# Kernel tuning notes

Hardware: AMD Instinct MI355X
Metric: run time of the kernel (lower is better)

The kernel has to match this reference:

```python
import jax, jax.numpy as jnp
import numpy as np

D_MODEL = 512
NUM_HEADS = 8
D_K = D_MODEL // NUM_HEADS
D_FF = 4 * D_MODEL
EPS = 1e-5


def _pos_encoding(seq_len, d_model, dtype=jnp.float32):
    pos = jnp.arange(seq_len, dtype=jnp.float32)[:, None]              # [S,1]
    div = jnp.exp(jnp.arange(0, d_model, 2, dtype=jnp.float32) * (-np.log(10000.0) / d_model))  # [D/2]
    ang = pos * div                                                      # [S,D/2]
    pe = jnp.stack([jnp.sin(ang), jnp.cos(ang)], axis=-1).reshape(seq_len, d_model)
    return pe.astype(dtype)


def _layernorm(x, g, b):
    mu = jnp.mean(x, axis=-1, keepdims=True)
    var = jnp.mean(jnp.square(x - mu), axis=-1, keepdims=True)
    return (x - mu) * jax.lax.rsqrt(var + EPS) * g + b


def setup_inputs() -> dict:
    key = jax.random.key(0)
    ks = jax.random.split(key, 12)
    B, S, D = 4, 2048, D_MODEL
    s = 1.0 / np.sqrt(D)
    inp = {
        "x": jax.random.normal(ks[0], (B, S, D), jnp.float32),
        "Wq": jax.random.normal(ks[1], (D, D), jnp.float32) * s,
        "bq": jnp.zeros((D,), jnp.float32),
        "Wk": jax.random.normal(ks[2], (D, D), jnp.float32) * s,
        "bk": jnp.zeros((D,), jnp.float32),
        "Wv": jax.random.normal(ks[3], (D, D), jnp.float32) * s,
        "bv": jnp.zeros((D,), jnp.float32),
        "Wo": jax.random.normal(ks[4], (D, D), jnp.float32) * s,
        "bo": jnp.zeros((D,), jnp.float32),
        "g1": jnp.ones((D,), jnp.float32),
        "b1": jnp.zeros((D,), jnp.float32),
        "W_ff1": jax.random.normal(ks[5], (D, D_FF), jnp.float32) * s,
        "b_ff1": jnp.zeros((D_FF,), jnp.float32),
        "W_ff2": jax.random.normal(ks[6], (D_FF, D), jnp.float32) * (1.0 / np.sqrt(D_FF)),
        "b_ff2": jnp.zeros((D,), jnp.float32),
        "g2": jnp.ones((D,), jnp.float32),
        "b2": jnp.zeros((D,), jnp.float32),
    }
    return inp


def reference(x, Wq, bq, Wk, bk, Wv, bv, Wo, bo, g1, b1, W_ff1, b_ff1, W_ff2, b_ff2, g2, b2):
    B, S, D = x.shape
    H, dk = NUM_HEADS, D_K
    # positional encoding (deterministic buffer)
    x = x + _pos_encoding(S, D, x.dtype)[None]
    # projections -> [B,H,S,dk]
    q = (x @ Wq + bq).reshape(B, S, H, dk).transpose(0, 2, 1, 3)
    k = (x @ Wk + bk).reshape(B, S, H, dk).transpose(0, 2, 1, 3)
    v = (x @ Wv + bv).reshape(B, S, H, dk).transpose(0, 2, 1, 3)
    # naive attention: materialized [B,H,S,S] scores (as in original)
    scores = jnp.einsum('bhqd,bhkd->bhqk', q, k) / np.sqrt(dk)
    attn = jax.nn.softmax(scores, axis=-1)
    ctx = jnp.einsum('bhqk,bhkd->bhqd', attn, v)
    ctx = ctx.transpose(0, 2, 1, 3).reshape(B, S, D)
    attn_out = ctx @ Wo + bo
    # residual + LN + FFN + residual + LN
    h = _layernorm(x + attn_out, g1, b1)
    ff = jax.nn.relu(h @ W_ff1 + b_ff1) @ W_ff2 + b_ff2
    return _layernorm(h + ff, g2, b2)
```

## Files before the change

### kernel.cpp

```cpp
#include <hip/hip_runtime.h>

typedef unsigned short u16;
typedef unsigned int u32;
typedef __attribute__((ext_vector_type(8))) short s16x8;
typedef __attribute__((ext_vector_type(2))) float f32x2;
typedef __attribute__((ext_vector_type(4))) float f32x4;
typedef __attribute__((ext_vector_type(16))) float f32x16;
typedef __attribute__((ext_vector_type(2))) u32 u32x2;
typedef __attribute__((ext_vector_type(4))) u32 u32x4;

#define MB (1ull << 20)
#define K1SCALE 0.18033688f

__device__ __forceinline__ u16 f2bf(float f) {
  u32 u = __float_as_uint(f);
  u32 r = (u + 0x7fffu + ((u >> 16) & 1u)) >> 16;
  return (u16)r;
}

__device__ __forceinline__ u32 cvtpk(float lo, float hi) {
  u32 r;
  asm("v_cvt_pk_bf16_f32 %0, %1, %2" : "=v"(r) : "v"(lo), "v"(hi));
  return r;
}

__device__ __forceinline__ f32x2 pk_add(f32x2 a, f32x2 b) {
  f32x2 d;
  asm("v_pk_add_f32 %0, %1, %2" : "=v"(d) : "v"(a), "v"(b));
  return d;
}

__device__ __forceinline__ void gload16(const u16* g, u16* l) {
  __builtin_amdgcn_global_load_lds((const __attribute__((address_space(1))) void*)g,
                                   (__attribute__((address_space(3))) void*)l, 16, 0, 0);
}

__global__ __launch_bounds__(256) void k_prep(const float* __restrict__ x,
                                              float* __restrict__ xf, u16* __restrict__ xb,
                                              const float* __restrict__ Wq, const float* __restrict__ Wk,
                                              const float* __restrict__ Wv, const float* __restrict__ Wo,
                                              const float* __restrict__ Wff1, const float* __restrict__ Wff2,
                                              const float* __restrict__ bq, const float* __restrict__ bk,
                                              const float* __restrict__ bv,
                                              u16* __restrict__ WqkvT, u16* __restrict__ WoT,
                                              u16* __restrict__ Wff1T, u16* __restrict__ Wff2T,
                                              float* __restrict__ bqkv) {
  __shared__ float tile[32][33];
  int bid = blockIdx.x;
  if (bid < 8192) {
    int idx = bid * 256 + threadIdx.x;
    int i2 = idx & 255;
    int srow = (idx >> 8) & 2047;
    float div = __expf((float)i2 * -0.03597789207803196f);
    float ang = (float)srow * div;
    f32x2 xv = *(const f32x2*)&x[(size_t)idx * 2];
    float v0 = xv[0] + __sinf(ang);
    float v1 = xv[1] + __cosf(ang);
    *(f32x2*)&xf[(size_t)idx * 2] = (f32x2){v0, v1};
    *(u32*)&xb[(size_t)idx * 2] = cvtpk(v0, v1);
    return;
  }
  int id = bid - 8192;
  if (id >= 3072) {
    int j = (id - 3072) * 256 + threadIdx.x;
    float v = (j < 512) ? bq[j] * K1SCALE : ((j < 1024) ? bk[j - 512] : bv[j - 1024]);
    bqkv[j] = v;
    return;
  }
  const float* W;
  u16* Wt;
  int K, N, k0, n0;
  float sc = 1.0f;
  if (id < 1024) {
    int mi = id >> 8, t = id & 255;
    K = 512; N = 512;
    k0 = (t & 15) * 32;
    n0 = (t >> 4) * 32;
    if (mi == 0) { W = Wq; Wt = WqkvT; sc = K1SCALE; }
    else if (mi == 1) { W = Wk; Wt = WqkvT + 512 * 512; }
    else if (mi == 2) { W = Wv; Wt = WqkvT + 2 * 512 * 512; }
    else { W = Wo; Wt = WoT; }
  } else if (id < 2048) {
    int t = id - 1024;
    K = 512; N = 2048;
    k0 = (t & 15) * 32;
    n0 = (t >> 4) * 32;
    W = Wff1; Wt = Wff1T;
  } else {
    int t = id - 2048;
    K = 2048; N = 512;
    k0 = (t >> 4) * 32;
    n0 = (t & 15) * 32;
    W = Wff2; Wt = Wff2T;
  }
  int tx = threadIdx.x & 31, ty = threadIdx.x >> 5;
  #pragma unroll
  for (int i = 0; i < 32; i += 8)
    tile[ty + i][tx] = W[(size_t)(k0 + ty + i) * N + n0 + tx];
  __syncthreads();
  #pragma unroll
  for (int i = 0; i < 32; i += 8)
    Wt[(size_t)(n0 + ty + i) * K + k0 + tx] = f2bf(tile[tx][ty + i] * sc);
}

template <int NK, bool RELU, bool QKV, bool F32OUT>
__global__ __launch_bounds__(512, 2) void k_gemm3(const u16* __restrict__ A, const u16* __restrict__ Bt,
                                                  const float* __restrict__ bias, u16* __restrict__ Cb,
                                                  u16* __restrict__ vTout,
                                                  float* __restrict__ Cf0, float* __restrict__ Cf1,
                                                  int N, int lda) {
  constexpr int K = NK * 64;
  __shared__ u16 lA[3][256 * 64];
  __shared__ u16 lB[3][128 * 64];
  int t = threadIdx.x;
  int lane = t & 63;
  int w = t >> 6;
  int wr = w >> 1, wc = w & 1;
  int g = lane >> 4, c = lane & 15;
  int nwg = gridDim.x * gridDim.y;
  int fid = blockIdx.y * gridDim.x + blockIdx.x;
  int wid = (fid & 7) * (nwg >> 3) + (fid >> 3);
  int bx = wid / gridDim.y;
  int by = wid % gridDim.y;
  size_t tm = (size_t)bx * 256;
  size_t tn = (size_t)by * 128;
  A += (size_t)blockIdx.z * K;
  Bt += (size_t)blockIdx.z * K;

  auto stg = [&](int buf, int kt, int half) {
    int k0 = kt * 64;
    #pragma unroll
    for (int i = 0; i < 2; i++) {
      int ch = t + (half * 2 + i) * 512;
      int row = ch >> 3;
      int koff = ((ch ^ row) & 7) << 3;
      gload16(A + (tm + row) * lda + k0 + koff, &lA[buf][ch * 8]);
    }
    int ch = t + half * 512;
    int row = ch >> 3;
    int koff = ((ch ^ row) & 7) << 3;
    gload16(Bt + (tn + row) * lda + k0 + koff, &lB[buf][ch * 8]);
  };

  f32x4 acc[4][4];
  #pragma unroll
  for (int i = 0; i < 4; i++)
    #pragma unroll
    for (int j = 0; j < 4; j++) acc[i][j] = (f32x4){0.f, 0.f, 0.f, 0.f};

  stg(0, 0, 0); stg(0, 0, 1);
  stg(1, 1, 0); stg(1, 1, 1);
  asm volatile("s_waitcnt vmcnt(6)" ::: "memory");
  __builtin_amdgcn_s_barrier();
  __builtin_amdgcn_sched_barrier(0);

  #pragma unroll
  for (int kt = 0; kt < NK; kt++) {
    const int buf = kt % 3;
    const int nb = (kt + 2) % 3;
    s16x8 bfr[4][2], afr[2][2];
    #pragma unroll
    for (int nr = 0; nr < 4; nr++)
      #pragma unroll
      for (int ks = 0; ks < 2; ks++)
        bfr[nr][ks] = *(const s16x8*)&lB[buf][(wc * 64 + nr * 16 + c) * 64 + (((g + 4 * ks) ^ (c & 7)) << 3)];
    #pragma unroll
    for (int mr = 0; mr < 2; mr++)
      #pragma unroll
      for (int ks = 0; ks < 2; ks++)
        afr[mr][ks] = *(const s16x8*)&lA[buf][(wr * 64 + mr * 16 + c) * 64 + (((g + 4 * ks) ^ (c & 7)) << 3)];
    if (kt + 2 < NK) stg(nb, kt + 2, 0);
    __builtin_amdgcn_s_barrier();
    __builtin_amdgcn_sched_barrier(0);
    __builtin_amdgcn_s_setprio(1);
    #pragma unroll
    for (int mr = 0; mr < 2; mr++)
      #pragma unroll
      for (int nr = 0; nr < 4; nr++)
        #pragma unroll
        for (int ks = 0; ks < 2; ks++)
          acc[mr][nr] = __builtin_amdgcn_mfma_f32_16x16x32_bf16(afr[mr][ks], bfr[nr][ks], acc[mr][nr], 0, 0, 0);
    __builtin_amdgcn_s_setprio(0);
    __builtin_amdgcn_s_barrier();
    __builtin_amdgcn_sched_barrier(0);
    #pragma unroll
    for (int mr = 0; mr < 2; mr++)
      #pragma unroll
      for (int ks = 0; ks < 2; ks++)
        afr[mr][ks] = *(const s16x8*)&lA[buf][(wr * 64 + (mr + 2) * 16 + c) * 64 + (((g + 4 * ks) ^ (c & 7)) << 3)];
    if (kt + 2 < NK) stg(nb, kt + 2, 1);
    __builtin_amdgcn_s_barrier();
    __builtin_amdgcn_sched_barrier(0);
    __builtin_amdgcn_s_setprio(1);
    #pragma unroll
    for (int mr = 0; mr < 2; mr++)
      #pragma unroll
      for (int nr = 0; nr < 4; nr++)
        #pragma unroll
        for (int ks = 0; ks < 2; ks++)
          acc[mr + 2][nr] = __builtin_amdgcn_mfma_f32_16x16x32_bf16(afr[mr][ks], bfr[nr][ks], acc[mr + 2][nr], 0, 0, 0);
    __builtin_amdgcn_s_setprio(0);
    if (kt < NK - 1) {
      if (kt + 2 < NK)
        asm volatile("s_waitcnt vmcnt(6)" ::: "memory");
      else
        asm volatile("s_waitcnt vmcnt(0)" ::: "memory");
      __builtin_amdgcn_s_barrier();
      __builtin_amdgcn_sched_barrier(0);
    }
  }

  if (QKV && tn >= 1024) {
    #pragma unroll
    for (int mr = 0; mr < 4; mr++) {
      int row0 = (int)tm + wr * 64 + mr * 16 + g * 4;
      int b = row0 >> 11, s0 = row0 & 2047;
      #pragma unroll
      for (int nr = 0; nr < 4; nr++) {
        int colr = (int)(tn - 1024) + wc * 64 + nr * 16 + c;
        int h = colr >> 6, d = colr & 63;
        float bv = bias[1024 + colr];
        u32 w0 = cvtpk(acc[mr][nr][0] + bv, acc[mr][nr][1] + bv);
        u32 w1 = cvtpk(acc[mr][nr][2] + bv, acc[mr][nr][3] + bv);
        u32x2 pp = {w0, w1};
        *(u32x2*)&vTout[((size_t)((b << 3) + h) * 64 + d) * 2048 + s0] = pp;
      }
    }
  } else if (F32OUT) {
    float* Cf = blockIdx.z ? Cf1 : Cf0;
    bool addb = (blockIdx.z == 0);
    #pragma unroll
    for (int nr = 0; nr < 4; nr++) {
      size_t col = tn + wc * 64 + nr * 16 + c;
      float bv = addb ? bias[col] : 0.0f;
      #pragma unroll
      for (int mr = 0; mr < 4; mr++) {
        size_t row0 = tm + wr * 64 + mr * 16 + g * 4;
        #pragma unroll
        for (int r = 0; r < 4; r++) Cf[(row0 + r) * N + col] = acc[mr][nr][r] + bv;
      }
    }
  } else {
    #pragma unroll
    for (int nr = 0; nr < 4; nr++) {
      size_t col = tn + wc * 64 + nr * 16 + c;
      float bv = bias[col];
      #pragma unroll
      for (int mr = 0; mr < 4; mr++) {
        size_t row0 = tm + wr * 64 + mr * 16 + g * 4;
        #pragma unroll
        for (int r = 0; r < 4; r++) {
          float v = acc[mr][nr][r] + bv;
          if (RELU) v = fmaxf(v, 0.0f);
          Cb[(row0 + r) * N + col] = f2bf(v);
        }
      }
    }
  }
}

template <int BN, bool RELU, bool WF32, bool WBF16>
__global__ __launch_bounds__(256) void k_gemm(const u16* __restrict__ A, const u16* __restrict__ Bt,
                                              const float* __restrict__ bias,
                                              float* __restrict__ Cf, u16* __restrict__ Cb,
                                              int N, int K) {
  constexpr int NACC = BN / 32;
  __shared__ u16 lA[128 * 64];
  __shared__ u16 lB[BN * 64];
  int t = threadIdx.x;
  int lane = t & 63;
  int w = t >> 6;
  int wm = w >> 1, wn = w & 1;
  int g = lane >> 4, c = lane & 15;
  int nwg = gridDim.x * gridDim.y;
  int fid = blockIdx.y * gridDim.x + blockIdx.x;
  int wid = (fid & 7) * (nwg >> 3) + (fid >> 3);
  int bx = wid / gridDim.y;
  int by = wid % gridDim.y;
  size_t tm = (size_t)bx * 128;
  size_t tn = (size_t)by * BN;

  f32x4 acc[4][NACC];
  #pragma unroll
  for (int i = 0; i < 4; i++)
    #pragma unroll
    for (int j = 0; j < NACC; j++) acc[i][j] = (f32x4){0.f, 0.f, 0.f, 0.f};

  for (int k0 = 0; k0 < K; k0 += 64) {
    __syncthreads();
    #pragma unroll
    for (int i = 0; i < 4; i++) {
      int ch = t + i * 256;
      int row = ch >> 3;
      int koff = ((ch ^ row) & 7) << 3;
      gload16(A + (tm + row) * K + k0 + koff, lA + ch * 8);
    }
    #pragma unroll
    for (int i = 0; i < BN / 32; i++) {
      int ch = t + i * 256;
      int row = ch >> 3;
      int koff = ((ch ^ row) & 7) << 3;
      gload16(Bt + (tn + row) * K + k0 + koff, lB + ch * 8);
    }
    __syncthreads();
    #pragma unroll
    for (int kh = 0; kh < 2; kh++) {
      int sl = ((g + 4 * kh) ^ (c & 7)) << 3;
      s16x8 af[4], bf[NACC];
      #pragma unroll
      for (int i = 0; i < 4; i++)
        af[i] = *(const s16x8*)&lA[(wm * 64 + i * 16 + c) * 64 + sl];
      #pragma unroll
      for (int j = 0; j < NACC; j++)
        bf[j] = *(const s16x8*)&lB[(wn * (BN / 2) + j * 16 + c) * 64 + sl];
      #pragma unroll
      for (int i = 0; i < 4; i++)
        #pragma unroll
        for (int j = 0; j < NACC; j++)
          acc[i][j] = __builtin_amdgcn_mfma_f32_16x16x32_bf16(af[i], bf[j], acc[i][j], 0, 0, 0);
    }
  }
  #pragma unroll
  for (int j = 0; j < NACC; j++) {
    size_t col = tn + wn * (BN / 2) + j * 16 + c;
    float bv = bias[col];
    #pragma unroll
    for (int i = 0; i < 4; i++) {
      size_t row0 = tm + wm * 64 + i * 16 + g * 4;
      #pragma unroll
      for (int r = 0; r < 4; r++) {
        float v = acc[i][j][r] + bv;
        if (RELU) v = fmaxf(v, 0.0f);
        if (WF32) Cf[(row0 + r) * N + col] = v;
        if (WBF16) Cb[(row0 + r) * N + col] = f2bf(v);
      }
    }
  }
}

union F16U {
  f32x16 v;
  f32x2 p[8];
};

__global__ __launch_bounds__(512, 4) void k_attn(const u16* __restrict__ qkv,
                                                 const u16* __restrict__ vT,
                                                 u16* __restrict__ ctx) {
  __shared__ u16 lds[8][4096];
  int t = threadIdx.x;
  int w = t >> 6, lane = t & 63;
  int qg = w >> 1, kh = w & 1;
  int ql = lane & 31, hi = lane >> 5;
  int bid = blockIdx.x;
  int wid = (bid & 7) * 64 + (bid >> 3);
  int bx = wid & 15;
  int bh = wid >> 4;
  int b = bh >> 3, h = bh & 7;
  int q0 = bx * 128 + qg * 32;
  int r7 = ql & 7;

  int sh = t >> 8;
  int th = t & 255;
  const u16* kbaseg = qkv + (size_t)(b * 2048 + sh * 1024) * 1536 + 512 + h * 64;
  const u16* vbaseg = vT + (size_t)(bh * 64) * 2048 + sh * 1024;

  auto stage = [&](int buf, int step) {
    int t0 = step * 64;
    #pragma unroll
    for (int i = 0; i < 2; i++) {
      int ch = th + i * 256;
      int row = ch >> 3;
      int off = ((ch ^ row) & 7) << 3;
      gload16(kbaseg + (size_t)(t0 + row) * 1536 + off, &lds[(sh * 2 + buf) * 2][ch * 8]);
      gload16(vbaseg + (size_t)row * 2048 + t0 + off, &lds[(sh * 2 + buf) * 2 + 1][ch * 8]);
    }
  };

  const u16* qbase = qkv + (size_t)(b * 2048 + q0 + ql) * 1536 + h * 64 + hi * 8;
  s16x8 qf[4];
  #pragma unroll
  for (int ks = 0; ks < 4; ks++) qf[ks] = *(const s16x8*)(qbase + ks * 16);

  float l = 0.f;
  F16U O0, O1;
  #pragma unroll
  for (int i = 0; i < 16; i++) { O0.v[i] = 0.f; O1.v[i] = 0.f; }

  stage(0, 0);

  for (int step = 0; step < 16; ++step) {
    int buf = step & 1;
    asm volatile("s_waitcnt vmcnt(0)" ::: "memory");
    __builtin_amdgcn_s_barrier();
    __builtin_amdgcn_sched_barrier(0);
    if (step < 15) stage(buf ^ 1, step + 1);

    const u16* lK = lds[(kh * 2 + buf) * 2];
    const u16* lV = lds[(kh * 2 + buf) * 2 + 1];

    F16U S0, S1;
    #pragma unroll
    for (int i = 0; i < 16; i++) { S0.v[i] = 0.f; S1.v[i] = 0.f; }
    #pragma unroll
    for (int ks = 0; ks < 4; ks++) {
      int so = ((ks * 2 + hi) ^ r7) << 3;
      s16x8 kf0 = *(const s16x8*)&lK[ql * 64 + so];
      s16x8 kf1 = *(const s16x8*)&lK[(32 + ql) * 64 + so];
      S0.v = __builtin_amdgcn_mfma_f32_32x32x16_bf16(kf0, qf[ks], S0.v, 0, 0, 0);
      S1.v = __builtin_amdgcn_mfma_f32_32x32x16_bf16(kf1, qf[ks], S1.v, 0, 0, 0);
    }

    #pragma unroll
    for (int i = 0; i < 16; i++) {
      S0.v[i] = __builtin_amdgcn_exp2f(S0.v[i]);
      S1.v[i] = __builtin_amdgcn_exp2f(S1.v[i]);
    }
    f32x2 c0 = pk_add(S0.p[0], S0.p[1]);
    f32x2 c1 = pk_add(S0.p[2], S0.p[3]);
    f32x2 c2 = pk_add(S0.p[4], S0.p[5]);
    f32x2 c3 = pk_add(S0.p[6], S0.p[7]);
    f32x2 d0 = pk_add(S1.p[0], S1.p[1]);
    f32x2 d1 = pk_add(S1.p[2], S1.p[3]);
    f32x2 d2 = pk_add(S1.p[4], S1.p[5]);
    f32x2 d3 = pk_add(S1.p[6], S1.p[7]);
    c0 = pk_add(c0, c1);
    c2 = pk_add(c2, c3);
    d0 = pk_add(d0, d1);
    d2 = pk_add(d2, d3);
    c0 = pk_add(c0, c2);
    d0 = pk_add(d0, d2);
    c0 = pk_add(c0, d0);
    float pssum = c0[0] + c0[1];
    pssum += __shfl_xor(pssum, 32, 64);
    l += pssum;

    auto pv = [&](const f32x16& sv, int kb) {
      u32 a0w = cvtpk(sv[0], sv[1]), a1w = cvtpk(sv[2], sv[3]);
      u32 a2w = cvtpk(sv[4], sv[5]), a3w = cvtpk(sv[6], sv[7]);
      u32 b0w = cvtpk(sv[8], sv[9]), b1w = cvtpk(sv[10], sv[11]);
      u32 b2w = cvtpk(sv[12], sv[13]), b3w = cvtpk(sv[14], sv[15]);
      asm("v_permlane32_swap_b32 %0, %1" : "+v"(a0w), "+v"(a2w));
      asm("v_permlane32_swap_b32 %0, %1" : "+v"(a1w), "+v"(a3w));
      asm("v_permlane32_swap_b32 %0, %1" : "+v"(b0w), "+v"(b2w));
      asm("v_permlane32_swap_b32 %0, %1" : "+v"(b1w), "+v"(b3w));
      u32x4 w0v = {a0w, a1w, a2w, a3w};
      u32x4 w1v = {b0w, b1w, b2w, b3w};
      s16x8 pf0 = __builtin_bit_cast(s16x8, w0v);
      s16x8 pf1 = __builtin_bit_cast(s16x8, w1v);
      int base0 = ((kb * 4 + hi) ^ r7) << 3;
      int base1 = ((kb * 4 + 2 + hi) ^ r7) << 3;
      s16x8 vf00 = *(const s16x8*)&lV[ql * 64 + base0];
      s16x8 vf01 = *(const s16x8*)&lV[ql * 64 + base1];
      s16x8 vf10 = *(const s16x8*)&lV[(32 + ql) * 64 + base0];
      s16x8 vf11 = *(const s16x8*)&lV[(32 + ql) * 64 + base1];
      O0.v = __builtin_amdgcn_mfma_f32_32x32x16_bf16(vf00, pf0, O0.v, 0, 0, 0);
      O0.v = __builtin_amdgcn_mfma_f32_32x32x16_bf16(vf01, pf1, O0.v, 0, 0, 0);
      O1.v = __builtin_amdgcn_mfma_f32_32x32x16_bf16(vf10, pf0, O1.v, 0, 0, 0);
      O1.v = __builtin_amdgcn_mfma_f32_32x32x16_bf16(vf11, pf1, O1.v, 0, 0, 0);
    };
    pv(S0.v, 0);
    pv(S1.v, 1);
  }

  asm volatile("s_waitcnt lgkmcnt(0)" ::: "memory");
  __builtin_amdgcn_s_barrier();
  float* mrg = (float*)&lds[0][0];
  float* p = mrg + (size_t)(qg * 64 + lane) * 34;
  if (kh == 1) {
    p[0] = l;
    #pragma unroll
    for (int i = 0; i < 16; i++) {
      p[1 + i] = O0.v[i];
      p[17 + i] = O1.v[i];
    }
  }
  asm volatile("s_waitcnt lgkmcnt(0)" ::: "memory");
  __builtin_amdgcn_s_barrier();
  if (kh == 0) {
    float inv = 1.0f / (l + p[0]);
    size_t obase = (size_t)(b * 2048 + q0 + ql) * 512 + h * 64;
    #pragma unroll
    for (int k = 0; k < 4; k++) {
      float v0 = (O0.v[4 * k] + p[1 + 4 * k]) * inv;
      float v1 = (O0.v[4 * k + 1] + p[1 + 4 * k + 1]) * inv;
      float v2 = (O0.v[4 * k + 2] + p[1 + 4 * k + 2]) * inv;
      float v3 = (O0.v[4 * k + 3] + p[1 + 4 * k + 3]) * inv;
      u32x2 p0 = {cvtpk(v0, v1), cvtpk(v2, v3)};
      *(u32x2*)&ctx[obase + 8 * k + 4 * hi] = p0;
      float u0 = (O1.v[4 * k] + p[17 + 4 * k]) * inv;
      float u1 = (O1.v[4 * k + 1] + p[17 + 4 * k + 1]) * inv;
      float u2 = (O1.v[4 * k + 2] + p[17 + 4 * k + 2]) * inv;
      float u3 = (O1.v[4 * k + 3] + p[17 + 4 * k + 3]) * inv;
      u32x2 p1 = {cvtpk(u0, u1), cvtpk(u2, u3)};
      *(u32x2*)&ctx[obase + 32 + 8 * k + 4 * hi] = p1;
    }
  }
}

template <bool WB>
__global__ __launch_bounds__(256) void k_addln(const float* __restrict__ A, const float* __restrict__ Bv,
                                               const float* __restrict__ G, const float* __restrict__ Bb,
                                               float* __restrict__ Of, u16* __restrict__ Ob) {
  int row = blockIdx.x;
  int t = threadIdx.x;
  size_t base = (size_t)row * 512 + 2 * t;
  f32x2 av = *(const f32x2*)&A[base];
  f32x2 bv = *(const f32x2*)&Bv[base];
  float x0 = av[0] + bv[0];
  float x1 = av[1] + bv[1];
  float s = x0 + x1;
  #pragma unroll
  for (int d = 1; d < 64; d <<= 1) s += __shfl_xor(s, d, 64);
  __shared__ float red[8];
  int w = t >> 6, lane = t & 63;
  if (lane == 0) red[w] = s;
  __syncthreads();
  float mu = (red[0] + red[1] + red[2] + red[3]) * (1.0f / 512.0f);
  float d0 = x0 - mu, d1 = x1 - mu;
  float vs = d0 * d0 + d1 * d1;
  #pragma unroll
  for (int d = 1; d < 64; d <<= 1) vs += __shfl_xor(vs, d, 64);
  if (lane == 0) red[4 + w] = vs;
  __syncthreads();
  float var = (red[4] + red[5] + red[6] + red[7]) * (1.0f / 512.0f);
  float rs = rsqrtf(var + 1e-5f);
  f32x2 gg = *(const f32x2*)&G[2 * t];
  f32x2 bb = *(const f32x2*)&Bb[2 * t];
  float o0 = d0 * rs * gg[0] + bb[0];
  float o1 = d1 * rs * gg[1] + bb[1];
  *(f32x2*)&Of[base] = (f32x2){o0, o1};
  if (WB) *(u32*)&Ob[base] = cvtpk(o0, o1);
}

__global__ __launch_bounds__(256) void k_addln3(const float* __restrict__ A, const float* __restrict__ B1,
                                                const float* __restrict__ B2,
                                                const float* __restrict__ G, const float* __restrict__ Bb,
                                                float* __restrict__ Of) {
  int row = blockIdx.x;
  int t = threadIdx.x;
  size_t base = (size_t)row * 512 + 2 * t;
  f32x2 av = *(const f32x2*)&A[base];
  f32x2 b1v = *(const f32x2*)&B1[base];
  f32x2 b2v = *(const f32x2*)&B2[base];
  float x0 = av[0] + b1v[0] + b2v[0];
  float x1 = av[1] + b1v[1] + b2v[1];
  float s = x0 + x1;
  #pragma unroll
  for (int d = 1; d < 64; d <<= 1) s += __shfl_xor(s, d, 64);
  __shared__ float red[8];
  int w = t >> 6, lane = t & 63;
  if (lane == 0) red[w] = s;
  __syncthreads();
  float mu = (red[0] + red[1] + red[2] + red[3]) * (1.0f / 512.0f);
  float d0 = x0 - mu, d1 = x1 - mu;
  float vs = d0 * d0 + d1 * d1;
  #pragma unroll
  for (int d = 1; d < 64; d <<= 1) vs += __shfl_xor(vs, d, 64);
  if (lane == 0) red[4 + w] = vs;
  __syncthreads();
  float var = (red[4] + red[5] + red[6] + red[7]) * (1.0f / 512.0f);
  float rs = rsqrtf(var + 1e-5f);
  f32x2 gg = *(const f32x2*)&G[2 * t];
  f32x2 bb = *(const f32x2*)&Bb[2 * t];
  float o0 = d0 * rs * gg[0] + bb[0];
  float o1 = d1 * rs * gg[1] + bb[1];
  *(f32x2*)&Of[base] = (f32x2){o0, o1};
}

extern "C" void kernel_launch(void* const* d_in, const int* in_sizes, int n_in,
                              void* d_out, int out_size, void* d_ws, size_t ws_size,
                              hipStream_t stream) {
  const float* x = (const float*)d_in[0];
  const float* Wq = (const float*)d_in[1];
  const float* bq = (const float*)d_in[2];
  const float* Wk = (const float*)d_in[3];
  const float* bk = (const float*)d_in[4];
  const float* Wv = (const float*)d_in[5];
  const float* bv = (const float*)d_in[6];
  const float* Wo = (const float*)d_in[7];
  const float* bo = (const float*)d_in[8];
  const float* g1 = (const float*)d_in[9];
  const float* b1 = (const float*)d_in[10];
  const float* Wff1 = (const float*)d_in[11];
  const float* bff1 = (const float*)d_in[12];
  const float* Wff2 = (const float*)d_in[13];
  const float* bff2 = (const float*)d_in[14];
  const float* g2 = (const float*)d_in[15];
  const float* b2 = (const float*)d_in[16];

  char* ws = (char*)d_ws;
  float* xpe_f = (float*)(ws + 0);
  float* ao2 = (float*)(ws + 0);
  u16* xpe_b = (u16*)(ws + 16 * MB);
  u16* qkv = (u16*)(ws + 24 * MB);
  u16* vT = (u16*)(ws + 48 * MB);
  u16* ctx = (u16*)(ws + 56 * MB);
  float* ao = (float*)(ws + 64 * MB);
  float* hf = (float*)(ws + 80 * MB);
  u16* hb = (u16*)(ws + 96 * MB);
  u16* ff1 = (u16*)(ws + 24 * MB);
  u16* WqkvT = (u16*)(ws + 104 * MB);
  u16* WoT = (u16*)(ws + 106 * MB);
  u16* Wff1T = (u16*)(ws + 107 * MB);
  u16* Wff2T = (u16*)(ws + 109 * MB);
  float* bqkv = (float*)(ws + 111 * MB);
  (void)in_sizes; (void)n_in; (void)out_size; (void)ws_size;

  k_prep<<<11270, 256, 0, stream>>>(x, xpe_f, xpe_b, Wq, Wk, Wv, Wo, Wff1, Wff2,
                                    bq, bk, bv, WqkvT, WoT, Wff1T, Wff2T, bqkv);

  k_gemm3<8, false, true, false><<<dim3(32, 12), 512, 0, stream>>>(xpe_b, WqkvT, bqkv, qkv, vT,
                                                                   nullptr, nullptr, 1536, 512);
  k_attn<<<512, 512, 0, stream>>>(qkv, vT, ctx);
  k_gemm<64, false, true, false><<<dim3(64, 8), 256, 0, stream>>>(ctx, WoT, bo, ao, nullptr, 512, 512);
  k_addln<true><<<8192, 256, 0, stream>>>(xpe_f, ao, g1, b1, hf, hb);
  k_gemm3<8, true, false, false><<<dim3(32, 16), 512, 0, stream>>>(hb, Wff1T, bff1, ff1, nullptr,
                                                                   nullptr, nullptr, 2048, 512);
  k_gemm3<16, false, false, true><<<dim3(32, 4, 2), 512, 0, stream>>>(ff1, Wff2T, bff2, nullptr, nullptr,
                                                                      ao, ao2, 512, 2048);
  k_addln3<<<8192, 256, 0, stream>>>(hf, ao, ao2, g2, b2, (float*)d_out);
}
```

Before: 171.5 us.

## Halve attention KV tile to 32 keys to cut LDS and raise occupancy

The attention kernel now stages 32 keys per step instead of 64, which halves the LDS tile and doubles the loop trip count. The V tile uses a new 4-slot XOR swizzle. The merge buffer drops its padding and keeps the row sums in a separate small array. With less LDS and fewer live score registers (one S accumulator instead of two), launch bounds rise from 4 to 6 blocks per CU to increase occupancy, at the cost of twice as many barriers and smaller transfers per step.

New measurement: 215.4 us. 1.26x slower.

```diff
diff --git a/kernel.cpp b/kernel.cpp
--- a/kernel.cpp
+++ b/kernel.cpp
@@ -343,10 +343,11 @@
   f32x2 p[8];
 };
 
-__global__ __launch_bounds__(512, 4) void k_attn(const u16* __restrict__ qkv,
+__global__ __launch_bounds__(512, 6) void k_attn(const u16* __restrict__ qkv,
                                                  const u16* __restrict__ vT,
                                                  u16* __restrict__ ctx) {
-  __shared__ u16 lds[8][4096];
+  __shared__ u16 lds[8][2048];
+  __shared__ float lml[256];
   int t = threadIdx.x;
   int w = t >> 6, lane = t & 63;
   int qg = w >> 1, kh = w & 1;
@@ -365,15 +366,13 @@
   const u16* vbaseg = vT + (size_t)(bh * 64) * 2048 + sh * 1024;
 
   auto stage = [&](int buf, int step) {
-    int t0 = step * 64;
-    #pragma unroll
-    for (int i = 0; i < 2; i++) {
-      int ch = th + i * 256;
-      int row = ch >> 3;
-      int off = ((ch ^ row) & 7) << 3;
-      gload16(kbaseg + (size_t)(t0 + row) * 1536 + off, &lds[(sh * 2 + buf) * 2][ch * 8]);
-      gload16(vbaseg + (size_t)row * 2048 + t0 + off, &lds[(sh * 2 + buf) * 2 + 1][ch * 8]);
-    }
+    int t0 = step * 32;
+    int krow = th >> 3;
+    int koff = ((th ^ krow) & 7) << 3;
+    gload16(kbaseg + (size_t)(t0 + krow) * 1536 + koff, &lds[(sh * 2 + buf) * 2][th * 8]);
+    int vrow = th >> 2;
+    int vslot = ((th & 3) ^ ((vrow >> 2) & 3)) & 3;
+    gload16(vbaseg + (size_t)vrow * 2048 + t0 + vslot * 8, &lds[(sh * 2 + buf) * 2 + 1][th * 8]);
   };
 
   const u16* qbase = qkv + (size_t)(b * 2048 + q0 + ql) * 1536 + h * 64 + hi * 8;
@@ -388,109 +387,93 @@
 
   stage(0, 0);
 
-  for (int step = 0; step < 16; ++step) {
+  for (int step = 0; step < 32; ++step) {
     int buf = step & 1;
     asm volatile("s_waitcnt vmcnt(0)" ::: "memory");
     __builtin_amdgcn_s_barrier();
     __builtin_amdgcn_sched_barrier(0);
-    if (step < 15) stage(buf ^ 1, step + 1);
+    if (step < 31) stage(buf ^ 1, step + 1);
 
     const u16* lK = lds[(kh * 2 + buf) * 2];
     const u16* lV = lds[(kh * 2 + buf) * 2 + 1];
 
-    F16U S0, S1;
-    #pragma unroll
-    for (int i = 0; i < 16; i++) { S0.v[i] = 0.f; S1.v[i] = 0.f; }
+    F16U S;
+    #pragma unroll
+    for (int i = 0; i < 16; i++) S.v[i] = 0.f;
     #pragma unroll
     for (int ks = 0; ks < 4; ks++) {
       int so = ((ks * 2 + hi) ^ r7) << 3;
-      s16x8 kf0 = *(const s16x8*)&lK[ql * 64 + so];
-      s16x8 kf1 = *(const s16x8*)&lK[(32 + ql) * 64 + so];
-      S0.v = __builtin_amdgcn_mfma_f32_32x32x16_bf16(kf0, qf[ks], S0.v, 0, 0, 0);
-      S1.v = __builtin_amdgcn_mfma_f32_32x32x16_bf16(kf1, qf[ks], S1.v, 0, 0, 0);
-    }
-
-    #pragma unroll
-    for (int i = 0; i < 16; i++) {
-      S0.v[i] = __builtin_amdgcn_exp2f(S0.v[i]);
-      S1.v[i] = __builtin_amdgcn_exp2f(S1.v[i]);
-    }
-    f32x2 c0 = pk_add(S0.p[0], S0.p[1]);
-    f32x2 c1 = pk_add(S0.p[2], S0.p[3]);
-    f32x2 c2 = pk_add(S0.p[4], S0.p[5]);
-    f32x2 c3 = pk_add(S0.p[6], S0.p[7]);
-    f32x2 d0 = pk_add(S1.p[0], S1.p[1]);
-    f32x2 d1 = pk_add(S1.p[2], S1.p[3]);
-    f32x2 d2 = pk_add(S1.p[4], S1.p[5]);
-    f32x2 d3 = pk_add(S1.p[6], S1.p[7]);
+      s16x8 kf = *(const s16x8*)&lK[ql * 64 + so];
+      S.v = __builtin_amdgcn_mfma_f32_32x32x16_bf16(kf, qf[ks], S.v, 0, 0, 0);
+    }
+
+    #pragma unroll
+    for (int i = 0; i < 16; i++) S.v[i] = __builtin_amdgcn_exp2f(S.v[i]);
+
+    f32x2 c0 = pk_add(S.p[0], S.p[1]);
+    f32x2 c1 = pk_add(S.p[2], S.p[3]);
+    f32x2 c2 = pk_add(S.p[4], S.p[5]);
+    f32x2 c3 = pk_add(S.p[6], S.p[7]);
     c0 = pk_add(c0, c1);
     c2 = pk_add(c2, c3);
-    d0 = pk_add(d0, d1);
-    d2 = pk_add(d2, d3);
     c0 = pk_add(c0, c2);
-    d0 = pk_add(d0, d2);
-    c0 = pk_add(c0, d0);
     float pssum = c0[0] + c0[1];
     pssum += __shfl_xor(pssum, 32, 64);
     l += pssum;
 
-    auto pv = [&](const f32x16& sv, int kb) {
-      u32 a0w = cvtpk(sv[0], sv[1]), a1w = cvtpk(sv[2], sv[3]);
-      u32 a2w = cvtpk(sv[4], sv[5]), a3w = cvtpk(sv[6], sv[7]);
-      u32 b0w = cvtpk(sv[8], sv[9]), b1w = cvtpk(sv[10], sv[11]);
-      u32 b2w = cvtpk(sv[12], sv[13]), b3w = cvtpk(sv[14], sv[15]);
-      asm("v_permlane32_swap_b32 %0, %1" : "+v"(a0w), "+v"(a2w));
-      asm("v_permlane32_swap_b32 %0, %1" : "+v"(a1w), "+v"(a3w));
-      asm("v_permlane32_swap_b32 %0, %1" : "+v"(b0w), "+v"(b2w));
-      asm("v_permlane32_swap_b32 %0, %1" : "+v"(b1w), "+v"(b3w));
-      u32x4 w0v = {a0w, a1w, a2w, a3w};
-      u32x4 w1v = {b0w, b1w, b2w, b3w};
-      s16x8 pf0 = __builtin_bit_cast(s16x8, w0v);
-      s16x8 pf1 = __builtin_bit_cast(s16x8, w1v);
-      int base0 = ((kb * 4 + hi) ^ r7) << 3;
-      int base1 = ((kb * 4 + 2 + hi) ^ r7) << 3;
-      s16x8 vf00 = *(const s16x8*)&lV[ql * 64 + base0];
-      s16x8 vf01 = *(const s16x8*)&lV[ql * 64 + base1];
-      s16x8 vf10 = *(const s16x8*)&lV[(32 + ql) * 64 + base0];
-      s16x8 vf11 = *(const s16x8*)&lV[(32 + ql) * 64 + base1];
-      O0.v = __builtin_amdgcn_mfma_f32_32x32x16_bf16(vf00, pf0, O0.v, 0, 0, 0);
-      O0.v = __builtin_amdgcn_mfma_f32_32x32x16_bf16(vf01, pf1, O0.v, 0, 0, 0);
-      O1.v = __builtin_amdgcn_mfma_f32_32x32x16_bf16(vf10, pf0, O1.v, 0, 0, 0);
-      O1.v = __builtin_amdgcn_mfma_f32_32x32x16_bf16(vf11, pf1, O1.v, 0, 0, 0);
-    };
-    pv(S0.v, 0);
-    pv(S1.v, 1);
+    u32 a0w = cvtpk(S.v[0], S.v[1]), a1w = cvtpk(S.v[2], S.v[3]);
+    u32 a2w = cvtpk(S.v[4], S.v[5]), a3w = cvtpk(S.v[6], S.v[7]);
+    u32 b0w = cvtpk(S.v[8], S.v[9]), b1w = cvtpk(S.v[10], S.v[11]);
+    u32 b2w = cvtpk(S.v[12], S.v[13]), b3w = cvtpk(S.v[14], S.v[15]);
+    asm("v_permlane32_swap_b32 %0, %1" : "+v"(a0w), "+v"(a2w));
+    asm("v_permlane32_swap_b32 %0, %1" : "+v"(a1w), "+v"(a3w));
+    asm("v_permlane32_swap_b32 %0, %1" : "+v"(b0w), "+v"(b2w));
+    asm("v_permlane32_swap_b32 %0, %1" : "+v"(b1w), "+v"(b3w));
+    u32x4 w0v = {a0w, a1w, a2w, a3w};
+    u32x4 w1v = {b0w, b1w, b2w, b3w};
+    s16x8 pf0 = __builtin_bit_cast(s16x8, w0v);
+    s16x8 pf1 = __builtin_bit_cast(s16x8, w1v);
+    #pragma unroll
+    for (int ks2 = 0; ks2 < 2; ks2++) {
+      int s0slot = ks2 * 2 + hi;
+      int r0 = ql, r1 = 32 + ql;
+      s16x8 vf0 = *(const s16x8*)&lV[r0 * 32 + (((s0slot) ^ ((r0 >> 2) & 3)) & 3) * 8];
+      s16x8 vf1 = *(const s16x8*)&lV[r1 * 32 + (((s0slot) ^ ((r1 >> 2) & 3)) & 3) * 8];
+      s16x8 pf = ks2 ? pf1 : pf0;
+      O0.v = __builtin_amdgcn_mfma_f32_32x32x16_bf16(vf0, pf, O0.v, 0, 0, 0);
+      O1.v = __builtin_amdgcn_mfma_f32_32x32x16_bf16(vf1, pf, O1.v, 0, 0, 0);
+    }
   }
 
   asm volatile("s_waitcnt lgkmcnt(0)" ::: "memory");
   __builtin_amdgcn_s_barrier();
   float* mrg = (float*)&lds[0][0];
-  float* p = mrg + (size_t)(qg * 64 + lane) * 34;
+  float* p = mrg + (size_t)(qg * 64 + lane) * 32;
   if (kh == 1) {
-    p[0] = l;
+    lml[qg * 64 + lane] = l;
     #pragma unroll
     for (int i = 0; i < 16; i++) {
-      p[1 + i] = O0.v[i];
-      p[17 + i] = O1.v[i];
+      p[i] = O0.v[i];
+      p[16 + i] = O1.v[i];
     }
   }
   asm volatile("s_waitcnt lgkmcnt(0)" ::: "memory");
   __builtin_amdgcn_s_barrier();
   if (kh == 0) {
-    float inv = 1.0f / (l + p[0]);
+    float inv = 1.0f / (l + lml[qg * 64 + lane]);
     size_t obase = (size_t)(b * 2048 + q0 + ql) * 512 + h * 64;
     #pragma unroll
     for (int k = 0; k < 4; k++) {
-      float v0 = (O0.v[4 * k] + p[1 + 4 * k]) * inv;
-      float v1 = (O0.v[4 * k + 1] + p[1 + 4 * k + 1]) * inv;
-      float v2 = (O0.v[4 * k + 2] + p[1 + 4 * k + 2]) * inv;
-      float v3 = (O0.v[4 * k + 3] + p[1 + 4 * k + 3]) * inv;
+      float v0 = (O0.v[4 * k] + p[4 * k]) * inv;
+      float v1 = (O0.v[4 * k + 1] + p[4 * k + 1]) * inv;
+      float v2 = (O0.v[4 * k + 2] + p[4 * k + 2]) * inv;
+      float v3 = (O0.v[4 * k + 3] + p[4 * k + 3]) * inv;
       u32x2 p0 = {cvtpk(v0, v1), cvtpk(v2, v3)};
       *(u32x2*)&ctx[obase + 8 * k + 4 * hi] = p0;
-      float u0 = (O1.v[4 * k] + p[17 + 4 * k]) * inv;
-      float u1 = (O1.v[4 * k + 1] + p[17 + 4 * k + 1]) * inv;
-      float u2 = (O1.v[4 * k + 2] + p[17 + 4 * k + 2]) * inv;
-      float u3 = (O1.v[4 * k + 3] + p[17 + 4 * k + 3]) * inv;
+      float u0 = (O1.v[4 * k] + p[16 + 4 * k]) * inv;
+      float u1 = (O1.v[4 * k + 1] + p[16 + 4 * k + 1]) * inv;
+      float u2 = (O1.v[4 * k + 2] + p[16 + 4 * k + 2]) * inv;
+      float u3 = (O1.v[4 * k + 3] + p[16 + 4 * k + 3]) * inv;
       u32x2 p1 = {cvtpk(u0, u1), cvtpk(u2, u3)};
       *(u32x2*)&ctx[obase + 32 + 8 * k + 4 * hi] = p1;
     }
```
